# Performance work log

Hardware: AMD Instinct MI355X
Metric: run time of the kernel (lower is better)

Reference implementation:

```python
import jax, jax.numpy as jnp
import numpy as np
from jax import lax

IMG_SIZE = 608
STRIDE = 32
NUM_CLASSES = 20
CONF_THRESH = 0.001
NMS_THRESH = 0.6
SLOPE = 0.1
B = 16
P5 = 512
FMP = IMG_SIZE // STRIDE   # 19
N = FMP * FMP              # 361 boxes per image


def _conv(x, w, b):
    y = lax.conv_general_dilated(x, w, (1, 1), 'SAME',
                                 dimension_numbers=('NCHW', 'OIHW', 'NCHW'))
    return y + b[None, :, None, None]


def _conv_act(x, w, b):
    # Conv block (conv + folded-BN bias + LeakyReLU(0.1)) at inference
    return jax.nn.leaky_relu(_conv(x, w, b), SLOPE)


def _grid():
    gy, gx = jnp.meshgrid(jnp.arange(FMP), jnp.arange(FMP), indexing='ij')
    return jnp.stack([gx, gy], axis=-1).reshape(-1, 2).astype(jnp.float32)  # [N,2]


def _decode(reg):
    # reg: [B,N,4] raw head output -> normalized x1y1x2y2 clamped to [0,1]
    xy = jax.nn.sigmoid(reg[..., :2]) + _grid()[None]          # center_sample=False
    wh = jnp.exp(reg[..., 2:])
    box = jnp.concatenate([xy - wh * 0.5, xy + wh * 0.5], axis=-1)
    return jnp.clip(box * (STRIDE / IMG_SIZE), 0.0, 1.0)


def _nms_one_class(boxes, s):
    # boxes: [N,4]; s: [N] scores with -1 marking boxes not of this class / below conf
    order = jnp.argsort(-s)
    b = boxes[order]
    valid = s[order] >= CONF_THRESH
    x1, y1, x2, y2 = b[:, 0], b[:, 1], b[:, 2], b[:, 3]
    areas = (x2 - x1) * (y2 - y1)
    w = jnp.maximum(1e-28, jnp.minimum(x2[:, None], x2[None, :]) - jnp.maximum(x1[:, None], x1[None, :]))
    h = jnp.maximum(1e-28, jnp.minimum(y2[:, None], y2[None, :]) - jnp.maximum(y1[:, None], y1[None, :]))
    inter = w * h
    iou = inter / (areas[:, None] + areas[None, :] - inter + 1e-14)  # [N,N]
    later = jnp.arange(N)[None, :] > jnp.arange(N)[:, None]
    sup = (iou > NMS_THRESH) & later

    def body(i, keep):
        # box i suppresses later boxes only if itself still kept (greedy NMS)
        return keep & ~(sup[i] & keep[i])

    keep = lax.fori_loop(0, N, body, valid)
    return jnp.zeros(N, dtype=bool).at[order].set(keep)  # back to original order


def _postprocess(boxes, scores):
    # per image: boxes [N,4], scores [N,C]
    cls_inds = jnp.argmax(scores, axis=-1)
    sc = jnp.max(scores, axis=-1)
    cmask = (cls_inds[None, :] == jnp.arange(NUM_CLASSES)[:, None]) & (sc >= CONF_THRESH)[None, :]
    masked = jnp.where(cmask, sc[None, :], -1.0)  # [C,N]
    keep_c = jax.vmap(_nms_one_class, in_axes=(None, 0))(boxes, masked)
    return sc, cls_inds, jnp.any(keep_c, axis=0)


def setup_inputs() -> dict:
    key = jax.random.key(0)
    ks = jax.random.split(key, 16)
    inp = {'x': jax.random.normal(ks[0], (B, P5, FMP, FMP), jnp.float32)}
    names = ['cls1', 'cls2', 'reg1', 'reg2', 'reg3', 'reg4']
    for j, nm in enumerate(names):
        inp['w_' + nm] = jax.random.normal(ks[1 + j], (P5, P5, 3, 3), jnp.float32) * 0.02
        inp['b_' + nm] = jnp.zeros((P5,), jnp.float32)
    inp['w_obj'] = jax.random.normal(ks[8], (1, P5, 1, 1), jnp.float32) * 0.01
    inp['b_obj'] = jnp.zeros((1,), jnp.float32)
    inp['w_clsh'] = jax.random.normal(ks[9], (NUM_CLASSES, P5, 1, 1), jnp.float32) * 0.01
    inp['b_clsh'] = jnp.zeros((NUM_CLASSES,), jnp.float32)
    inp['w_regh'] = jax.random.normal(ks[10], (4, P5, 1, 1), jnp.float32) * 0.01
    inp['b_regh'] = jnp.zeros((4,), jnp.float32)
    return inp


def reference(x, w_cls1, b_cls1, w_cls2, b_cls2, w_reg1, b_reg1, w_reg2, b_reg2,
              w_reg3, b_reg3, w_reg4, b_reg4, w_obj, b_obj, w_clsh, b_clsh,
              w_regh, b_regh):
    cf = _conv_act(_conv_act(x, w_cls1, b_cls1), w_cls2, b_cls2)
    rf = x
    for wv, bv in ((w_reg1, b_reg1), (w_reg2, b_reg2), (w_reg3, b_reg3), (w_reg4, b_reg4)):
        rf = _conv_act(rf, wv, bv)

    def flat(t):  # [B,C,H,W] -> [B,N,C]
        return t.reshape(t.shape[0], t.shape[1], -1).transpose(0, 2, 1)

    obj = flat(_conv(rf, w_obj, b_obj))      # [B,N,1]
    clsp = flat(_conv(cf, w_clsh, b_clsh))   # [B,N,C]
    regp = flat(_conv(rf, w_regh, b_regh))   # [B,N,4]

    boxes = _decode(regp)                                        # [B,N,4]
    scores = jax.nn.sigmoid(obj) * jax.nn.softmax(clsp, axis=-1)  # [B,N,C]
    sc, cls_inds, keep = jax.vmap(_postprocess)(boxes, scores)
    # fixed-shape outputs: boxes [B,N,4], per-box best score [B,N],
    # class index [B,N], NMS keep mask [B,N]
    return boxes, sc, cls_inds, keep
```

## Files before the change

### kernel.cpp

```cpp
#include <hip/hip_runtime.h>
#include <hip/hip_bf16.h>
#include <stdint.h>

typedef __bf16 bf16x8 __attribute__((ext_vector_type(8)));
typedef float  f32x16 __attribute__((ext_vector_type(16)));

#define FMPX 19
#define NPOS 361
#define CCH  512
#define NB   16
#define NCLS 20
#define CONF_T 0.001f
#define NMS_TH 0.6f
#define BSCALE (32.0f/608.0f)

#define SC_OFF   (NB*NPOS*4)
#define CLS_OFF  (SC_OFF + NB*NPOS)
#define KEEP_OFF (CLS_OFF + NB*NPOS)

#define GSTR  3528
#define PLANE ((size_t)3612672)
#define WSL   294912
#define XBUF  16384
#define WBUF  18432
#define WOFF  32768
#define SMEMB 69632

__device__ __forceinline__ void gl_lds16(const void* g, void* l) {
  __builtin_amdgcn_global_load_lds(
      (const __attribute__((address_space(1))) unsigned int*)g,
      (__attribute__((address_space(3))) unsigned int*)l, 16, 0, 0);
}
#define MFMA32(A,B,C) __builtin_amdgcn_mfma_f32_32x32x16_bf16(A,B,C,0,0,0)
#define SG(m,n) __builtin_amdgcn_sched_group_barrier(m, n, 0)
#define PRIO1 __builtin_amdgcn_s_setprio(1)
#define PRIO0 __builtin_amdgcn_s_setprio(0)

__global__ void split_x_k(const float* __restrict__ x, __bf16* __restrict__ Xd) {
  __shared__ float sx[8][368];
  int g = blockIdx.x, b = blockIdx.y;
  int tid = threadIdx.x;
  for (int i = tid; i < 8*361; i += 256) {
    int ci = i / 361, p = i - ci*361;
    sx[ci][p] = x[((size_t)b*CCH + g*8 + ci)*NPOS + p];
  }
  __syncthreads();
  for (int row = tid; row < 441; row += 256) {
    int y = row/21, xx = row - y*21;
    bf16x8 oh = {}, om = {};
    if (y >= 1 && y <= 19 && xx >= 1 && xx <= 19) {
      int p = (y-1)*19 + xx - 1;
#pragma unroll
      for (int j = 0; j < 8; ++j) {
        float v = sx[j][p];
        __bf16 hh = (__bf16)v;
        oh[j] = hh; om[j] = (__bf16)(v - (float)hh);
      }
    }
    size_t o = (((size_t)b)*64 + g)*GSTR + (size_t)row*8;
    *(bf16x8*)(Xd + o)         = oh;
    *(bf16x8*)(Xd + PLANE + o) = om;
  }
}

__global__ void repack_k(const float* __restrict__ w, __bf16* __restrict__ Wg) {
  __shared__ float sw[32][145];
  int slice = blockIdx.x, chunk = blockIdx.y;
  int tid = threadIdx.x;
  for (int i = tid; i < 32*144; i += 256) {
    int cl = i / 144, r = i - cl*144;
    sw[cl][r] = w[((size_t)slice*32 + cl)*4608 + chunk*144 + r];
  }
  __syncthreads();
  for (int u = tid; u < 1152; u += 256) {
    int co = u & 31, kh = (u >> 5) & 1, pt = u >> 6;
    int tap = pt % 9, pl = pt / 9;
    bf16x8 o;
#pragma unroll
    for (int j = 0; j < 8; ++j) {
      float v = sw[co][(kh*8 + j)*9 + tap];
      __bf16 hh = (__bf16)v;
      o[j] = pl == 0 ? hh : (__bf16)(v - (float)hh);
    }
    *(bf16x8*)(Wg + (((size_t)(slice*2 + pl)*9 + tap)*32 + chunk)*512 + kh*256 + co*8) = o;
  }
}

#define RD6X(SP, AT, IMM) do { \
  SP##0 = *(const bf16x8*)(Xc + AT##0 + (IMM)); \
  SP##1 = *(const bf16x8*)(Xc + AT##1 + (IMM)); \
  SP##2 = *(const bf16x8*)(Xc + AT##2 + (IMM)); \
  SP##3 = *(const bf16x8*)(Xc + AT##3 + (IMM)); \
  SP##4 = *(const bf16x8*)(Xc + AT##4 + (IMM)); \
  SP##5 = *(const bf16x8*)(Xc + AT##5 + (IMM)); } while (0)

#define CL(SP, BH_, BM_) do { \
  acc0 = MFMA32(SP##0, BH_, acc0); acc1 = MFMA32(SP##1, BH_, acc1); \
  acc2 = MFMA32(SP##2, BH_, acc2); acc3 = MFMA32(SP##3, BH_, acc3); \
  acc4 = MFMA32(SP##4, BH_, acc4); acc5 = MFMA32(SP##5, BH_, acc5); \
  acc0 = MFMA32(SP##0, BM_, acc0); acc1 = MFMA32(SP##1, BM_, acc1); \
  acc2 = MFMA32(SP##2, BM_, acc2); acc3 = MFMA32(SP##3, BM_, acc3); \
  acc4 = MFMA32(SP##4, BM_, acc4); acc5 = MFMA32(SP##5, BM_, acc5); } while (0)

#define CLH(SP, B_) do { \
  acc0 = MFMA32(SP##0, B_, acc0); acc1 = MFMA32(SP##1, B_, acc1); \
  acc2 = MFMA32(SP##2, B_, acc2); acc3 = MFMA32(SP##3, B_, acc3); \
  acc4 = MFMA32(SP##4, B_, acc4); acc5 = MFMA32(SP##5, B_, acc5); } while (0)

#define STO(A, MTL) do { _Pragma("unroll") \
  for (int r = 0; r < 16; ++r) { \
    Lf[wq*3552 + ((MTL)*32 + 4*kh + (r & 3) + 8*(r >> 2))*37 + col] = (A)[r]; } } while (0)

__global__ __launch_bounds__(256, 2) void conv3x3_mfma(
    const __bf16* __restrict__ Xs, const __bf16* __restrict__ Wg,
    const float* __restrict__ bias, __bf16* __restrict__ Xd)
{
  __shared__ __attribute__((aligned(16))) char smem[SMEMB];
  const int tid = threadIdx.x;
  const int bid = blockIdx.x;
  const int b = bid & 15, slice = (bid >> 4) & 15, h = bid >> 8;
  const int lane = tid & 63;
  const int wq = __builtin_amdgcn_readfirstlane(tid >> 6);
  const int col = lane & 31, kh = lane >> 5;
  const int kh4096 = kh*4096;
  const int PB = h*190, CNT = h ? 171 : 190;
  const int PEND = PB + CNT - 1;
  const int clampU = h ? 230 : 251;

  int ab0, ab1, ab2, ab3, ab4, ab5;
  {
    int ao[6];
#pragma unroll
    for (int mt = 0; mt < 6; ++mt) {
      int p = PB + mt*32 + col; if (p > PEND) p = PEND;
      int pp = p + 2*(p/19) + 22;
      ao[mt] = (pp - h*210)*16;
    }
    ab0 = ao[0]; ab1 = ao[1]; ab2 = ao[2]; ab3 = ao[3]; ab4 = ao[4]; ab5 = ao[5];
  }
  const int boff = kh*512 + col*16;

  const int goffs[9] = {-352,-336,-320,-16,0,16,320,336,352};
  const int t0 = 2*wq, t1 = t0 + 1;
  const int g0 = goffs[t0], g1 = goffs[t1];
  const int a8im = 352 + ((wq & 2) ? 8192 : 0);
  const int t0a0 = ab0+g0, t0a1 = ab1+g0, t0a2 = ab2+g0,
            t0a3 = ab3+g0, t0a4 = ab4+g0, t0a5 = ab5+g0;
  const int t1a0 = ab0+g1, t1a1 = ab1+g1, t1a2 = ab2+g1,
            t1a3 = ab3+g1, t1a4 = ab4+g1, t1a5 = ab5+g1;
  const int t8a0 = ab0+a8im, t8a1 = ab1+a8im, t8a2 = ab2+a8im,
            t8a3 = ab3+a8im, t8a4 = ab4+a8im, t8a5 = ab5+a8im;
  const int wb0 = t0*1024 + boff, wb1 = t1*1024 + boff;
  const int wb8 = 8192 + boff + ((wq & 1) ? 9216 : 0);

  int ux = wq*64 + lane; if (ux > clampU) ux = clampU;
  const __bf16* xsb = Xs + (size_t)b*64*GSTR + (size_t)(h*210 + ux)*8;
  const __bf16* wsb = Wg + (size_t)slice*WSL + (size_t)lane*8;
  int wsrc0, wsrc1, wsrc2, wsrc3, wsrc4;
  int wdst0, wdst1, wdst2, wdst3, wdst4;
  {
    int ws[5], wd[5];
#pragma unroll
    for (int q = 0; q < 5; ++q) {
      int wk = (wq*5 + q) % 18;
      int pl = wk > 8 ? 1 : 0, tap = wk - 9*pl;
      ws[q] = ((pl*9 + tap)*32)*512;
      wd[q] = WOFF + pl*9216 + tap*1024;
    }
    wsrc0 = ws[0]; wsrc1 = ws[1]; wsrc2 = ws[2]; wsrc3 = ws[3]; wsrc4 = ws[4];
    wdst0 = wd[0]; wdst1 = wd[1]; wdst2 = wd[2]; wdst3 = wd[3]; wdst4 = wd[4];
  }

  auto stage = [&](int c1, int buf) {
    const __bf16* xs = xsb + (size_t)(2*c1)*GSTR;
    char* xd = smem + (buf ? XBUF : 0) + wq*1024;
    gl_lds16(xs,                    xd);
    gl_lds16(xs + GSTR,             xd + 4096);
    gl_lds16(xs + PLANE,            xd + 8192);
    gl_lds16(xs + PLANE + GSTR,     xd + 12288);
    const __bf16* wsc = wsb + (size_t)c1*512;
    char* wb = smem + (buf ? WBUF : 0);
    gl_lds16(wsc + wsrc0, wb + wdst0);
    gl_lds16(wsc + wsrc1, wb + wdst1);
    gl_lds16(wsc + wsrc2, wb + wdst2);
    gl_lds16(wsc + wsrc3, wb + wdst3);
    gl_lds16(wsc + wsrc4, wb + wdst4);
  };

  f32x16 acc0 = {}, acc1 = {}, acc2 = {}, acc3 = {}, acc4 = {}, acc5 = {};

  stage(0, 0);
  __syncthreads();

  for (int c = 0; c < 32; ++c) {
    const char* Xc = smem + (c & 1)*XBUF + kh4096;
    const char* Wc = smem + WOFF + (c & 1)*WBUF;
    const int cn = (c < 31) ? (c + 1) : 31;

    bf16x8 Aa0, Aa1, Aa2, Aa3, Aa4, Aa5;
    bf16x8 Ab0, Ab1, Ab2, Ab3, Ab4, Ab5;
    bf16x8 Ac0, Ac1, Ac2, Ac3, Ac4, Ac5;
    bf16x8 B0h, B0m, B1h, B1m, B8v;

    RD6X(Aa, t0a, 0);
    B0h = *(const bf16x8*)(Wc + wb0);
    B0m = *(const bf16x8*)(Wc + wb0 + 9216);
    RD6X(Ab, t0a, 8192);
    stage(cn, (c + 1) & 1);
    PRIO1;
    RD6X(Ac, t1a, 0);
    B1h = *(const bf16x8*)(Wc + wb1);
    B1m = *(const bf16x8*)(Wc + wb1 + 9216);
    CL(Aa, B0h, B0m);
    RD6X(Aa, t1a, 8192);
    CL(Ab, B0h, B0m);
    RD6X(Ab, t8a, 0);
    B8v = *(const bf16x8*)(Wc + wb8);
    CL(Ac, B1h, B1m);
    CL(Aa, B1h, B1m);
    CLH(Ab, B8v);
    PRIO0;

    SG(0x100, 14);
    SG(0x70, 9);
#pragma unroll
    for (int i = 0; i < 4; ++i) { SG(8, 3); SG(0x100, 2); }
#pragma unroll
    for (int i = 0; i < 6; ++i) { SG(8, 2); SG(0x100, 1); }
#pragma unroll
    for (int i = 0; i < 7; ++i) { SG(8, 1); SG(0x100, 1); }
    SG(8, 5);
    SG(8, 18);
    __syncthreads();
  }

  float* Lf = (float*)smem;
#pragma unroll
  for (int half = 0; half < 2; ++half) {
    if (half == 0) { STO(acc0, 0); STO(acc1, 1); STO(acc2, 2); }
    else           { STO(acc3, 0); STO(acc4, 1); STO(acc5, 2); }
    __syncthreads();
    for (int u = tid; u < 768; u += 256) {
      int pl = u / 384, rem = u - pl*384;
      int gq = rem / 96, lp = rem - gq*96;
      int lpos = half*96 + lp;
      if (lpos < CNT) {
        int p = PB + lpos;
        int pp = p + 2*(p/19) + 22;
        const float* bb = bias + slice*32 + gq*8;
        bf16x8 o;
#pragma unroll
        for (int j = 0; j < 8; ++j) {
          int coix = lp*37 + gq*8 + j;
          float v = Lf[coix] + Lf[3552 + coix] + Lf[7104 + coix] + Lf[10656 + coix] + bb[j];
          v = v > 0.f ? v : 0.1f*v;
          __bf16 hh = (__bf16)v;
          o[j] = pl == 0 ? hh : (__bf16)(v - (float)hh);
        }
        *(bf16x8*)(Xd + (((size_t)pl*16 + b)*64 + slice*4 + gq)*GSTR + (size_t)pp*8) = o;
      }
    }
    __syncthreads();
  }

  const int nh = h ? 39 : 41;
  for (int u = tid; u < 8*nh; u += 256) {
    int pl = u / (4*nh); int rem = u - pl*4*nh;
    int gq = rem / nh; int ci2 = rem - gq*nh;
    int rowpos;
    if (ci2 < 21) rowpos = h ? (420 + ci2) : ci2;
    else { int q = ci2 - 21; rowpos = ((h ? 11 : 1) + (q >> 1))*21 + 20*(q & 1); }
    bf16x8 z = {};
    *(bf16x8*)(Xd + (((size_t)pl*16 + b)*64 + slice*4 + gq)*GSTR + (size_t)rowpos*8) = z;
  }
}

__global__ __launch_bounds__(256) void head_rf_k(
    const __bf16* __restrict__ F, const float* __restrict__ wobj,
    const float* __restrict__ bobj, const float* __restrict__ wreg,
    const float* __restrict__ breg, float* __restrict__ obj, float* __restrict__ regp)
{
  int gw = blockIdx.x*4 + (threadIdx.x >> 6);
  if (gw >= NB*NPOS) return;
  int lane = threadIdx.x & 63;
  int b = gw / NPOS, p = gw % NPOS;
  int pp = p + 2*(p/19) + 22;
  const __bf16* base = F + (((size_t)b)*64 + lane)*GSTR + (size_t)pp*8;
  bf16x8 v0 = *(const bf16x8*)base;
  bf16x8 v1 = *(const bf16x8*)(base + PLANE);
  float f[8];
#pragma unroll
  for (int j = 0; j < 8; ++j) f[j] = (float)v0[j] + (float)v1[j];
#pragma unroll
  for (int o = 0; o < 5; ++o) {
    const float* wp = (o == 0) ? wobj : wreg + (o-1)*CCH;
    float4 wa = *(const float4*)(wp + lane*8);
    float4 wb = *(const float4*)(wp + lane*8 + 4);
    float s2 = f[0]*wa.x + f[1]*wa.y + f[2]*wa.z + f[3]*wa.w
             + f[4]*wb.x + f[5]*wb.y + f[6]*wb.z + f[7]*wb.w;
#pragma unroll
    for (int d = 32; d; d >>= 1) s2 += __shfl_xor(s2, d);
    if (lane == 0) {
      if (o == 0) obj[gw] = s2 + bobj[0];
      else regp[(size_t)gw*4 + (o-1)] = s2 + breg[o-1];
    }
  }
}

__global__ __launch_bounds__(256) void head_cls_k(
    const __bf16* __restrict__ F, const float* __restrict__ wcls,
    const float* __restrict__ bcls, float* __restrict__ clsp)
{
  int gw = blockIdx.x*4 + (threadIdx.x >> 6);
  if (gw >= NB*NPOS) return;
  int lane = threadIdx.x & 63;
  int b = gw / NPOS, p = gw % NPOS;
  int pp = p + 2*(p/19) + 22;
  const __bf16* base = F + (((size_t)b)*64 + lane)*GSTR + (size_t)pp*8;
  bf16x8 v0 = *(const bf16x8*)base;
  bf16x8 v1 = *(const bf16x8*)(base + PLANE);
  float f[8];
#pragma unroll
  for (int j = 0; j < 8; ++j) f[j] = (float)v0[j] + (float)v1[j];
#pragma unroll
  for (int o = 0; o < NCLS; ++o) {
    const float* wp = wcls + o*CCH;
    float4 wa = *(const float4*)(wp + lane*8);
    float4 wb = *(const float4*)(wp + lane*8 + 4);
    float s2 = f[0]*wa.x + f[1]*wa.y + f[2]*wa.z + f[3]*wa.w
             + f[4]*wb.x + f[5]*wb.y + f[6]*wb.z + f[7]*wb.w;
#pragma unroll
    for (int d = 32; d; d >>= 1) s2 += __shfl_xor(s2, d);
    if (lane == 0) clsp[(size_t)gw*NCLS + o] = s2 + bcls[o];
  }
}

__global__ void decode_k(const float* __restrict__ obj, const float* __restrict__ clsp,
                         const float* __restrict__ regp, float* __restrict__ outb)
{
  int i = blockIdx.x * 256 + threadIdx.x;
  if (i >= NB * NPOS) return;
  int p = i % NPOS;
  float gx = (float)(p % FMPX), gy = (float)(p / FMPX);
  float4 rg = *(const float4*)&regp[(size_t)i * 4];
  float cx = 1.f / (1.f + expf(-rg.x)) + gx;
  float cy = 1.f / (1.f + expf(-rg.y)) + gy;
  float whw = expf(rg.z), whh = expf(rg.w);
  float x1 = fminf(fmaxf((cx - whw * 0.5f) * BSCALE, 0.f), 1.f);
  float y1 = fminf(fmaxf((cy - whh * 0.5f) * BSCALE, 0.f), 1.f);
  float x2 = fminf(fmaxf((cx + whw * 0.5f) * BSCALE, 0.f), 1.f);
  float y2 = fminf(fmaxf((cy + whh * 0.5f) * BSCALE, 0.f), 1.f);
  outb[(size_t)i * 4 + 0] = x1; outb[(size_t)i * 4 + 1] = y1;
  outb[(size_t)i * 4 + 2] = x2; outb[(size_t)i * 4 + 3] = y2;

  float so = 1.f / (1.f + expf(-obj[i]));
  float cv[20];
  const float4* cp = (const float4*)&clsp[(size_t)i * 20];
#pragma unroll
  for (int q = 0; q < 5; q++) {
    float4 v4 = cp[q];
    cv[q * 4] = v4.x; cv[q * 4 + 1] = v4.y; cv[q * 4 + 2] = v4.z; cv[q * 4 + 3] = v4.w;
  }
  float mx = cv[0];
#pragma unroll
  for (int c = 1; c < 20; c++) mx = fmaxf(mx, cv[c]);
  float sum = 0.f;
#pragma unroll
  for (int c = 0; c < 20; c++) { cv[c] = expf(cv[c] - mx); sum += cv[c]; }
  float inv = so / sum;
  float best = -1.f; int bi = 0;
#pragma unroll
  for (int c = 0; c < 20; c++) { float s = cv[c] * inv; if (s > best) { best = s; bi = c; } }
  outb[SC_OFF + i] = best;
  outb[CLS_OFF + i] = (float)bi;
  outb[KEEP_OFF + i] = 0.f;
}

__device__ inline unsigned ordf(float f) {
  unsigned u = __float_as_uint(f);
  return (u & 0x80000000u) ? ~u : (u | 0x80000000u);
}

__global__ __launch_bounds__(64) void nms_k(const float* __restrict__ outb, float* __restrict__ keep_out)
{
  int b = blockIdx.x / NCLS, c = blockIdx.x % NCLS;
  int lane = threadIdx.x;
  __shared__ unsigned long long keys[512];
  __shared__ float bx1[384], by1[384], bx2[384], by2[384], bar[384];
  __shared__ unsigned kp[384];
  __shared__ int sj[384];

  for (int i = lane; i < 512; i += 64) {
    unsigned long long key = 0ULL;
    if (i < NPOS) {
      float sc = outb[SC_OFF + b * NPOS + i];
      int ci = (int)outb[CLS_OFF + b * NPOS + i];
      float s = (ci == c && sc >= CONF_T) ? sc : -1.0f;
      key = ((unsigned long long)ordf(s) << 32) | (unsigned)(~(unsigned)i);
    }
    keys[i] = key;
  }
  __syncthreads();
  for (int kk = 2; kk <= 512; kk <<= 1) {
    for (int jj = kk >> 1; jj > 0; jj >>= 1) {
      for (int i = lane; i < 512; i += 64) {
        int l2 = i ^ jj;
        if (l2 > i) {
          unsigned long long a = keys[i], bb2 = keys[l2];
          bool dir = (i & kk) == 0;
          bool sw = dir ? (a < bb2) : (a > bb2);
          if (sw) { keys[i] = bb2; keys[l2] = a; }
        }
      }
      __syncthreads();
    }
  }
  unsigned ordc = ordf(CONF_T);
  int nvalid = 0;
  for (int i = lane; i < 384; i += 64) {
    unsigned long long key = keys[i];
    unsigned hi = (unsigned)(key >> 32);
    int j = (int)(~(unsigned)key);
    bool valid = (key != 0ULL) && (hi >= ordc);
    kp[i] = valid ? 1u : 0u;
    if (valid) {
      const float* bp = &outb[(size_t)(b * NPOS + j) * 4];
      float x1 = bp[0], y1 = bp[1], x2 = bp[2], y2 = bp[3];
      bx1[i] = x1; by1[i] = y1; bx2[i] = x2; by2[i] = y2;
      bar[i] = (x2 - x1) * (y2 - y1);
      sj[i] = j;
    } else { bx1[i] = 0; by1[i] = 0; bx2[i] = 0; by2[i] = 0; bar[i] = 0; sj[i] = 0; }
    nvalid += __popcll(__ballot(valid));
  }
  __syncthreads();
  for (int i = 0; i < nvalid; ++i) {
    if (kp[i]) {
      float x1i = bx1[i], y1i = by1[i], x2i = bx2[i], y2i = by2[i], ai = bar[i];
      for (int j2 = i + 1 + lane; j2 < nvalid; j2 += 64) {
        if (kp[j2]) {
          float ww = fmaxf(1e-28f, fminf(x2i, bx2[j2]) - fmaxf(x1i, bx1[j2]));
          float hh = fmaxf(1e-28f, fminf(y2i, by2[j2]) - fmaxf(y1i, by1[j2]));
          float inter = ww * hh;
          float iou = inter / (ai + bar[j2] - inter + 1e-14f);
          if (iou > NMS_TH) kp[j2] = 0u;
        }
      }
    }
    __syncthreads();
  }
  for (int i = lane; i < 384; i += 64)
    if (kp[i]) keep_out[b * NPOS + sj[i]] = 1.0f;
}

extern "C" void kernel_launch(void* const* d_in, const int* in_sizes, int n_in,
                              void* d_out, int out_size, void* d_ws, size_t ws_size,
                              hipStream_t stream)
{
  const float* x      = (const float*)d_in[0];
  const float* w_cls1 = (const float*)d_in[1];  const float* b_cls1 = (const float*)d_in[2];
  const float* w_cls2 = (const float*)d_in[3];  const float* b_cls2 = (const float*)d_in[4];
  const float* w_reg1 = (const float*)d_in[5];  const float* b_reg1 = (const float*)d_in[6];
  const float* w_reg2 = (const float*)d_in[7];  const float* b_reg2 = (const float*)d_in[8];
  const float* w_reg3 = (const float*)d_in[9];  const float* b_reg3 = (const float*)d_in[10];
  const float* w_reg4 = (const float*)d_in[11]; const float* b_reg4 = (const float*)d_in[12];
  const float* w_obj  = (const float*)d_in[13]; const float* b_obj  = (const float*)d_in[14];
  const float* w_clsh = (const float*)d_in[15]; const float* b_clsh = (const float*)d_in[16];
  const float* w_regh = (const float*)d_in[17]; const float* b_regh = (const float*)d_in[18];
  float* outb = (float*)d_out;

  __bf16* Xs0 = (__bf16*)d_ws;
  __bf16* XsA = Xs0 + 2*PLANE;
  __bf16* XsB = XsA + 2*PLANE;
  __bf16* Wg  = XsB + 2*PLANE;
  float* obj  = (float*)(Wg + (size_t)16*WSL);
  float* regp = obj + NB*NPOS;
  float* clsp = regp + (size_t)NB*NPOS*4;

  auto conv = [&](const float* wsrc, const float* bsrc, const __bf16* src, __bf16* dst) {
    repack_k<<<dim3(16, 32), 256, 0, stream>>>(wsrc, Wg);
    conv3x3_mfma<<<512, 256, 0, stream>>>(src, Wg, bsrc, dst);
  };

  split_x_k<<<dim3(64, NB), 256, 0, stream>>>(x, Xs0);
  conv(w_reg1, b_reg1, Xs0, XsA);
  conv(w_reg2, b_reg2, XsA, XsB);
  conv(w_reg3, b_reg3, XsB, XsA);
  conv(w_reg4, b_reg4, XsA, XsB);
  head_rf_k<<<1444, 256, 0, stream>>>(XsB, w_obj, b_obj, w_regh, b_regh, obj, regp);
  conv(w_cls1, b_cls1, Xs0, XsA);
  conv(w_cls2, b_cls2, XsA, XsB);
  head_cls_k<<<1444, 256, 0, stream>>>(XsB, w_clsh, b_clsh, clsp);
  decode_k<<<(NB * NPOS + 255) / 256, 256, 0, stream>>>(obj, clsp, regp, outb);
  nms_k<<<NB * NCLS, 64, 0, stream>>>(outb, outb + KEEP_OFF);
}
```

Baseline: 679.0 us.

## Split conv spatial work into three blocks with single-buffered weights for occupancy

The conv kernel now tiles the 361 positions into three pieces of 128/128/105 positions (4 M-tiles instead of 6), launching 768 blocks instead of 512. The weight LDS buffer goes from double to single buffering, with an extra barrier after the weight fragments are read, which shrinks LDS to about 50KB and the launch bound rises to 3 blocks per CU. The aim is higher occupancy and better spread across CUs. In exchange there is an extra sync per channel chunk, more redundant halo loads of the input, and the halo-row zeroing is handled by the h==0 block alone.

```diff
diff --git a/kernel.cpp b/kernel.cpp
--- a/kernel.cpp
+++ b/kernel.cpp
@@ -22,9 +22,8 @@
 #define PLANE ((size_t)3612672)
 #define WSL   294912
 #define XBUF  16384
-#define WBUF  18432
 #define WOFF  32768
-#define SMEMB 69632
+#define SMEMB 51200
 
 __device__ __forceinline__ void gl_lds16(const void* g, void* l) {
   __builtin_amdgcn_global_load_lds(
@@ -86,32 +85,27 @@
   }
 }
 
-#define RD6X(SP, AT, IMM) do { \
+#define RD4X(SP, AT, IMM) do { \
   SP##0 = *(const bf16x8*)(Xc + AT##0 + (IMM)); \
   SP##1 = *(const bf16x8*)(Xc + AT##1 + (IMM)); \
   SP##2 = *(const bf16x8*)(Xc + AT##2 + (IMM)); \
-  SP##3 = *(const bf16x8*)(Xc + AT##3 + (IMM)); \
-  SP##4 = *(const bf16x8*)(Xc + AT##4 + (IMM)); \
-  SP##5 = *(const bf16x8*)(Xc + AT##5 + (IMM)); } while (0)
-
-#define CL(SP, BH_, BM_) do { \
+  SP##3 = *(const bf16x8*)(Xc + AT##3 + (IMM)); } while (0)
+
+#define CL4(SP, BH_, BM_) do { \
   acc0 = MFMA32(SP##0, BH_, acc0); acc1 = MFMA32(SP##1, BH_, acc1); \
   acc2 = MFMA32(SP##2, BH_, acc2); acc3 = MFMA32(SP##3, BH_, acc3); \
-  acc4 = MFMA32(SP##4, BH_, acc4); acc5 = MFMA32(SP##5, BH_, acc5); \
   acc0 = MFMA32(SP##0, BM_, acc0); acc1 = MFMA32(SP##1, BM_, acc1); \
-  acc2 = MFMA32(SP##2, BM_, acc2); acc3 = MFMA32(SP##3, BM_, acc3); \
-  acc4 = MFMA32(SP##4, BM_, acc4); acc5 = MFMA32(SP##5, BM_, acc5); } while (0)
-
-#define CLH(SP, B_) do { \
+  acc2 = MFMA32(SP##2, BM_, acc2); acc3 = MFMA32(SP##3, BM_, acc3); } while (0)
+
+#define CL4H(SP, B_) do { \
   acc0 = MFMA32(SP##0, B_, acc0); acc1 = MFMA32(SP##1, B_, acc1); \
-  acc2 = MFMA32(SP##2, B_, acc2); acc3 = MFMA32(SP##3, B_, acc3); \
-  acc4 = MFMA32(SP##4, B_, acc4); acc5 = MFMA32(SP##5, B_, acc5); } while (0)
+  acc2 = MFMA32(SP##2, B_, acc2); acc3 = MFMA32(SP##3, B_, acc3); } while (0)
 
 #define STO(A, MTL) do { _Pragma("unroll") \
   for (int r = 0; r < 16; ++r) { \
-    Lf[wq*3552 + ((MTL)*32 + 4*kh + (r & 3) + 8*(r >> 2))*37 + col] = (A)[r]; } } while (0)
-
-__global__ __launch_bounds__(256, 2) void conv3x3_mfma(
+    Lf[wq*2368 + ((MTL)*32 + 4*kh + (r & 3) + 8*(r >> 2))*37 + col] = (A)[r]; } } while (0)
+
+__global__ __launch_bounds__(256, 3) void conv3x3_mfma(
     const __bf16* __restrict__ Xs, const __bf16* __restrict__ Wg,
     const float* __restrict__ bias, __bf16* __restrict__ Xd)
 {
@@ -123,20 +117,21 @@
   const int wq = __builtin_amdgcn_readfirstlane(tid >> 6);
   const int col = lane & 31, kh = lane >> 5;
   const int kh4096 = kh*4096;
-  const int PB = h*190, CNT = h ? 171 : 190;
+  const int PB = h*128, CNT = (h == 2) ? 105 : 128;
   const int PEND = PB + CNT - 1;
-  const int clampU = h ? 230 : 251;
-
-  int ab0, ab1, ab2, ab3, ab4, ab5;
+  const int wstart = (h == 0) ? 0 : (h == 1) ? 140 : 282;
+  const int clampU = (h == 2) ? 158 : 255;
+
+  int ab0, ab1, ab2, ab3;
   {
-    int ao[6];
-#pragma unroll
-    for (int mt = 0; mt < 6; ++mt) {
+    int ao[4];
+#pragma unroll
+    for (int mt = 0; mt < 4; ++mt) {
       int p = PB + mt*32 + col; if (p > PEND) p = PEND;
       int pp = p + 2*(p/19) + 22;
-      ao[mt] = (pp - h*210)*16;
-    }
-    ab0 = ao[0]; ab1 = ao[1]; ab2 = ao[2]; ab3 = ao[3]; ab4 = ao[4]; ab5 = ao[5];
+      ao[mt] = (pp - wstart)*16;
+    }
+    ab0 = ao[0]; ab1 = ao[1]; ab2 = ao[2]; ab3 = ao[3];
   }
   const int boff = kh*512 + col*16;
 
@@ -144,17 +139,14 @@
   const int t0 = 2*wq, t1 = t0 + 1;
   const int g0 = goffs[t0], g1 = goffs[t1];
   const int a8im = 352 + ((wq & 2) ? 8192 : 0);
-  const int t0a0 = ab0+g0, t0a1 = ab1+g0, t0a2 = ab2+g0,
-            t0a3 = ab3+g0, t0a4 = ab4+g0, t0a5 = ab5+g0;
-  const int t1a0 = ab0+g1, t1a1 = ab1+g1, t1a2 = ab2+g1,
-            t1a3 = ab3+g1, t1a4 = ab4+g1, t1a5 = ab5+g1;
-  const int t8a0 = ab0+a8im, t8a1 = ab1+a8im, t8a2 = ab2+a8im,
-            t8a3 = ab3+a8im, t8a4 = ab4+a8im, t8a5 = ab5+a8im;
+  const int t0a0 = ab0+g0, t0a1 = ab1+g0, t0a2 = ab2+g0, t0a3 = ab3+g0;
+  const int t1a0 = ab0+g1, t1a1 = ab1+g1, t1a2 = ab2+g1, t1a3 = ab3+g1;
+  const int t8a0 = ab0+a8im, t8a1 = ab1+a8im, t8a2 = ab2+a8im, t8a3 = ab3+a8im;
   const int wb0 = t0*1024 + boff, wb1 = t1*1024 + boff;
   const int wb8 = 8192 + boff + ((wq & 1) ? 9216 : 0);
 
   int ux = wq*64 + lane; if (ux > clampU) ux = clampU;
-  const __bf16* xsb = Xs + (size_t)b*64*GSTR + (size_t)(h*210 + ux)*8;
+  const __bf16* xsb = Xs + (size_t)b*64*GSTR + (size_t)(wstart + ux)*8;
   const __bf16* wsb = Wg + (size_t)slice*WSL + (size_t)lane*8;
   int wsrc0, wsrc1, wsrc2, wsrc3, wsrc4;
   int wdst0, wdst1, wdst2, wdst3, wdst4;
@@ -179,71 +171,69 @@
     gl_lds16(xs + PLANE,            xd + 8192);
     gl_lds16(xs + PLANE + GSTR,     xd + 12288);
     const __bf16* wsc = wsb + (size_t)c1*512;
-    char* wb = smem + (buf ? WBUF : 0);
-    gl_lds16(wsc + wsrc0, wb + wdst0);
-    gl_lds16(wsc + wsrc1, wb + wdst1);
-    gl_lds16(wsc + wsrc2, wb + wdst2);
-    gl_lds16(wsc + wsrc3, wb + wdst3);
-    gl_lds16(wsc + wsrc4, wb + wdst4);
+    gl_lds16(wsc + wsrc0, smem + wdst0);
+    gl_lds16(wsc + wsrc1, smem + wdst1);
+    gl_lds16(wsc + wsrc2, smem + wdst2);
+    gl_lds16(wsc + wsrc3, smem + wdst3);
+    gl_lds16(wsc + wsrc4, smem + wdst4);
   };
 
-  f32x16 acc0 = {}, acc1 = {}, acc2 = {}, acc3 = {}, acc4 = {}, acc5 = {};
+  f32x16 acc0 = {}, acc1 = {}, acc2 = {}, acc3 = {};
 
   stage(0, 0);
   __syncthreads();
 
   for (int c = 0; c < 32; ++c) {
     const char* Xc = smem + (c & 1)*XBUF + kh4096;
-    const char* Wc = smem + WOFF + (c & 1)*WBUF;
+    const char* Wc = smem + WOFF;
     const int cn = (c < 31) ? (c + 1) : 31;
 
-    bf16x8 Aa0, Aa1, Aa2, Aa3, Aa4, Aa5;
-    bf16x8 Ab0, Ab1, Ab2, Ab3, Ab4, Ab5;
-    bf16x8 Ac0, Ac1, Ac2, Ac3, Ac4, Ac5;
-    bf16x8 B0h, B0m, B1h, B1m, B8v;
-
-    RD6X(Aa, t0a, 0);
-    B0h = *(const bf16x8*)(Wc + wb0);
-    B0m = *(const bf16x8*)(Wc + wb0 + 9216);
-    RD6X(Ab, t0a, 8192);
+    bf16x8 B0h = *(const bf16x8*)(Wc + wb0);
+    bf16x8 B0m = *(const bf16x8*)(Wc + wb0 + 9216);
+    bf16x8 B1h = *(const bf16x8*)(Wc + wb1);
+    bf16x8 B1m = *(const bf16x8*)(Wc + wb1 + 9216);
+    bf16x8 B8v = *(const bf16x8*)(Wc + wb8);
+    __syncthreads();
+
     stage(cn, (c + 1) & 1);
+
+    bf16x8 Aa0, Aa1, Aa2, Aa3;
+    bf16x8 Ab0, Ab1, Ab2, Ab3;
     PRIO1;
-    RD6X(Ac, t1a, 0);
-    B1h = *(const bf16x8*)(Wc + wb1);
-    B1m = *(const bf16x8*)(Wc + wb1 + 9216);
-    CL(Aa, B0h, B0m);
-    RD6X(Aa, t1a, 8192);
-    CL(Ab, B0h, B0m);
-    RD6X(Ab, t8a, 0);
-    B8v = *(const bf16x8*)(Wc + wb8);
-    CL(Ac, B1h, B1m);
-    CL(Aa, B1h, B1m);
-    CLH(Ab, B8v);
+    RD4X(Aa, t0a, 0);
+    RD4X(Ab, t0a, 8192);
+    CL4(Aa, B0h, B0m);
+    RD4X(Aa, t1a, 0);
+    CL4(Ab, B0h, B0m);
+    RD4X(Ab, t1a, 8192);
+    CL4(Aa, B1h, B1m);
+    RD4X(Aa, t8a, 0);
+    CL4(Ab, B1h, B1m);
+    CL4H(Aa, B8v);
     PRIO0;
 
-    SG(0x100, 14);
+    SG(0x100, 8);
     SG(0x70, 9);
 #pragma unroll
-    for (int i = 0; i < 4; ++i) { SG(8, 3); SG(0x100, 2); }
-#pragma unroll
-    for (int i = 0; i < 6; ++i) { SG(8, 2); SG(0x100, 1); }
-#pragma unroll
-    for (int i = 0; i < 7; ++i) { SG(8, 1); SG(0x100, 1); }
-    SG(8, 5);
-    SG(8, 18);
+    for (int i = 0; i < 4; ++i) { SG(8, 2); SG(0x100, 1); }
+#pragma unroll
+    for (int i = 0; i < 4; ++i) { SG(8, 2); SG(0x100, 1); }
+#pragma unroll
+    for (int i = 0; i < 4; ++i) { SG(8, 2); SG(0x100, 1); }
+    SG(8, 12);
     __syncthreads();
   }
 
   float* Lf = (float*)smem;
 #pragma unroll
   for (int half = 0; half < 2; ++half) {
-    if (half == 0) { STO(acc0, 0); STO(acc1, 1); STO(acc2, 2); }
-    else           { STO(acc3, 0); STO(acc4, 1); STO(acc5, 2); }
+    if (half == 0) { STO(acc0, 0); STO(acc1, 1); }
+    else           { STO(acc2, 0); STO(acc3, 1); }
     __syncthreads();
-    for (int u = tid; u < 768; u += 256) {
-      int pl = u / 384, rem = u - pl*384;
-      int gq = rem / 96, lp = rem - gq*96;
-      int lpos = half*96 + lp;
+    for (int u = tid; u < 512; u += 256) {
+      int pl = u / 256, rem = u - pl*256;
+      int gq = rem / 64, lp = rem - gq*64;
+      int lpos = half*64 + lp;
       if (lpos < CNT) {
         int p = PB + lpos;
         int pp = p + 2*(p/19) + 22;
@@ -252,7 +242,7 @@
 #pragma unroll
         for (int j = 0; j < 8; ++j) {
           int coix = lp*37 + gq*8 + j;
-          float v = Lf[coix] + Lf[3552 + coix] + Lf[7104 + coix] + Lf[10656 + coix] + bb[j];
+          float v = Lf[coix] + Lf[2368 + coix] + Lf[4736 + coix] + Lf[7104 + coix] + bb[j];
           v = v > 0.f ? v : 0.1f*v;
           __bf16 hh = (__bf16)v;
           o[j] = pl == 0 ? hh : (__bf16)(v - (float)hh);
@@ -263,15 +253,17 @@
     __syncthreads();
   }
 
-  const int nh = h ? 39 : 41;
-  for (int u = tid; u < 8*nh; u += 256) {
-    int pl = u / (4*nh); int rem = u - pl*4*nh;
-    int gq = rem / nh; int ci2 = rem - gq*nh;
-    int rowpos;
-    if (ci2 < 21) rowpos = h ? (420 + ci2) : ci2;
-    else { int q = ci2 - 21; rowpos = ((h ? 11 : 1) + (q >> 1))*21 + 20*(q & 1); }
-    bf16x8 z = {};
-    *(bf16x8*)(Xd + (((size_t)pl*16 + b)*64 + slice*4 + gq)*GSTR + (size_t)rowpos*8) = z;
+  if (h == 0) {
+    for (int u = tid; u < 8*80; u += 256) {
+      int pl = u / 320; int rem = u - pl*320;
+      int gq = rem / 80; int ci2 = rem - gq*80;
+      int rowpos;
+      if (ci2 < 21) rowpos = ci2;
+      else if (ci2 < 42) rowpos = 420 + (ci2 - 21);
+      else { int q = ci2 - 42; rowpos = (1 + (q >> 1))*21 + 20*(q & 1); }
+      bf16x8 z = {};
+      *(bf16x8*)(Xd + (((size_t)pl*16 + b)*64 + slice*4 + gq)*GSTR + (size_t)rowpos*8) = z;
+    }
   }
 }
 
@@ -478,7 +470,7 @@
 
   auto conv = [&](const float* wsrc, const float* bsrc, const __bf16* src, __bf16* dst) {
     repack_k<<<dim3(16, 32), 256, 0, stream>>>(wsrc, Wg);
-    conv3x3_mfma<<<512, 256, 0, stream>>>(src, Wg, bsrc, dst);
+    conv3x3_mfma<<<768, 256, 0, stream>>>(src, Wg, bsrc, dst);
   };
 
   split_x_k<<<dim3(64, NB), 256, 0, stream>>>(x, Xs0);
```

Result: slower. 710.9 us (+4.7%).
